# Kernel optimization log

Measured on AMD Instinct MI355X. Metric: run time of the kernel, lower is better.

The kernel has to match this reference:

```python
import jax, jax.numpy as jnp
import numpy as np

EMB_TABLE = 80000  # full shared embedding rows
N_ITEMS = 50000    # target item count (item_num + 1)
E = 600000         # edges
D = 128            # embedding_size
L = 3              # num_gcn_layers


def gcn_conv(x, W, b, src, dst, norm, n):
    # PyG GCNConv: x' = lin(x); out[i] = sum_{(j->i)} norm_ji * x'[j] + bias
    msgs = (x @ W)[src] * norm[:, None]          # [E+n, D]
    out = jax.ops.segment_sum(msgs, dst, num_segments=n)
    return out + b


def setup_inputs() -> dict:
    key = jax.random.key(0)
    k0, k1, k2 = jax.random.split(key, 3)
    item_emb = jax.random.normal(k0, (EMB_TABLE, D), dtype=jnp.float32) * 0.02
    weights = jax.random.normal(k1, (L, D, D), dtype=jnp.float32) * (1.0 / np.sqrt(D))
    biases = jnp.zeros((L, D), dtype=jnp.float32)
    edge_index = jax.random.randint(k2, (2, E), 0, N_ITEMS, dtype=jnp.int64)
    return {"item_emb": item_emb, "weights": weights, "biases": biases,
            "edge_index": edge_index, "item_nums": N_ITEMS}


def reference(item_emb, weights, biases, edge_index, item_nums):
    n = item_nums
    x0 = item_emb[-n:]  # embeds[0] = item_emb[-item_nums:]
    loops = jnp.arange(n, dtype=edge_index.dtype)
    src = jnp.concatenate([edge_index[0], loops])  # add self-loops (GCNConv default)
    dst = jnp.concatenate([edge_index[1], loops])
    # symmetric normalization: deg computed on target side with self-loops
    deg = jax.ops.segment_sum(jnp.ones_like(src, dtype=x0.dtype), dst, num_segments=n)
    dinv = jnp.where(deg > 0, jax.lax.rsqrt(jnp.maximum(deg, 1e-12)), 0.0)
    norm = dinv[src] * dinv[dst]                   # [E+n]
    embeds = [x0]
    for l in range(weights.shape[0]):
        embeds.append(gcn_conv(embeds[-1], weights[l], biases[l], src, dst, norm, n))
    total = embeds[0]
    for e in embeds[1:]:
        total = total + e
    return (total, *embeds)
```

## Files before the change

kernel.cpp:

```cpp
#include <hip/hip_runtime.h>
#include <stdint.h>

#define D 128

typedef unsigned int u32;
typedef unsigned short u16;
typedef __attribute__((ext_vector_type(8))) short short8;
typedef __attribute__((ext_vector_type(4))) float f32x4;

static __device__ __forceinline__ float bf2f(u16 h) {
    return __uint_as_float(((u32)h) << 16);
}
static __device__ __forceinline__ u16 f2bf(float f) {
    u32 u = __float_as_uint(f);
    u32 r = (u + 0x7fffu + ((u >> 16) & 1u)) >> 16;
    return (u16)r;
}
static __device__ __forceinline__ int clampi(int v, int n) {
    if (v < 0) v = 0;
    if (v >= n) v = n - 1;
    return v;
}

__global__ void k_init(int* __restrict__ hist, int* __restrict__ csr_pos, int n,
                       const u16* __restrict__ emb_raw, const u32* __restrict__ ei_raw,
                       const u16* __restrict__ w_raw, int* __restrict__ flags) {
    int i = blockIdx.x * 256 + threadIdx.x;
    if (i < n) {
        hist[i] = 0;
        csr_pos[i] = 0;
    }
    if (blockIdx.x == 0 && threadIdx.x < 64) {
        int t = threadIdx.x;
        int se = 0, sw = 0, zz = 0;
#pragma unroll
        for (int q = 0; q < 4; q++) {
            int k = t * 4 + q;
            u16 he = emb_raw[2 * k];
            u32 exe = (he >> 7) & 0xFF;
            if (he == 0 || (exe >= 0x60 && exe <= 0x8F)) se++;
            u16 hw = w_raw[2 * k];
            u32 exw = (hw >> 7) & 0xFF;
            if (hw == 0 || (exw >= 0x60 && exw <= 0x8F)) sw++;
            if (ei_raw[2 * k + 1] == 0) zz++;
        }
#pragma unroll
        for (int o = 32; o; o >>= 1) {
            se += __shfl_down(se, o);
            sw += __shfl_down(sw, o);
            zz += __shfl_down(zz, o);
        }
        if (t == 0) {
            flags[0] = (se >= 200) ? 1 : 0;
            flags[2] = (sw >= 200) ? 1 : 0;
            flags[1] = (zz >= 200) ? 1 : 0;
        }
    }
}

__global__ __launch_bounds__(256) void k_wprep(const void* __restrict__ Wbase,
                                               const int* __restrict__ flags,
                                               u16* __restrict__ WB) {
    int idx = blockIdx.x * 256 + threadIdx.x;
    int e = idx & 7;
    int l = (idx >> 3) & 63;
    int ks = (idx >> 9) & 3;
    int c = (idx >> 11) & 7;
    int layer = idx >> 14;
    int k = ks * 32 + ((l >> 4) << 3) + e;
    int j = (c << 4) + (l & 15);
    size_t src = (size_t)layer * D * D + (size_t)k * D + j;
    float w = flags[2] ? bf2f(((const u16*)Wbase)[src]) : ((const float*)Wbase)[src];
    u16 hb = f2bf(w);
    u16 lb = f2bf(w - bf2f(hb));
    size_t o = (size_t)layer * 32768 + (size_t)((c * 4 + ks) * 64 + l) * 8 + e;
    WB[o] = hb;
    WB[o + 16384] = lb;
}

__global__ void k_hist(const u32* __restrict__ ei, int E, int n,
                       const int* __restrict__ flags, int* __restrict__ hist) {
    int e = blockIdx.x * 256 + threadIdx.x;
    if (e >= E) return;
    int d;
    if (flags[1]) d = ((const int2*)ei)[(size_t)E + e].x;
    else          d = (int)ei[(size_t)E + e];
    atomicAdd(&hist[clampi(d, n)], 1);
}

__global__ void k_scan1(const int* __restrict__ hist, int n,
                        int* __restrict__ incl, int* __restrict__ bsums) {
    __shared__ int s[256];
    int t = threadIdx.x;
    int i = blockIdx.x * 256 + t;
    int v = (i < n) ? hist[i] : 0;
    s[t] = v;
    __syncthreads();
    for (int d2 = 1; d2 < 256; d2 <<= 1) {
        int add = (t >= d2) ? s[t - d2] : 0;
        __syncthreads();
        s[t] += add;
        __syncthreads();
    }
    if (i < n) incl[i] = s[t];
    if (t == 255) bsums[blockIdx.x] = s[255];
}

__global__ void k_scan23(const int* __restrict__ hist, const int* __restrict__ bsums,
                         int n, int* __restrict__ csr_off, float* __restrict__ dinv) {
    __shared__ int s[256];
    int t = threadIdx.x, b = blockIdx.x;
    s[t] = (t < b) ? bsums[t] : 0;
    __syncthreads();
    for (int o = 128; o; o >>= 1) {
        if (t < o) s[t] += s[t + o];
        __syncthreads();
    }
    int add = s[0];
    int i = b * 256 + t;
    if (i < n) {
        int h = hist[i];
        csr_off[i] = add + csr_off[i] - h;
        dinv[i] = rsqrtf((float)(h + 1));
    }
}

__global__ void k_sx(const u32* __restrict__ ei, int E, int n,
                     const int* __restrict__ flags,
                     const int* __restrict__ csr_off, int* __restrict__ csr_pos,
                     const float* __restrict__ dinv, int2* __restrict__ csr_pair,
                     const void* __restrict__ emb, int off_elems, int nD4,
                     float* __restrict__ out_x0, int eb) {
    int bid = blockIdx.x;
    if (bid < eb) {
        int e = bid * 256 + threadIdx.x;
        if (e >= E) return;
        int s, d;
        if (flags[1]) {
            s = ((const int2*)ei)[e].x;
            d = ((const int2*)ei)[(size_t)E + e].x;
        } else {
            s = (int)ei[e];
            d = (int)ei[(size_t)E + e];
        }
        s = clampi(s, n);
        d = clampi(d, n);
        int p = csr_off[d] + atomicAdd(&csr_pos[d], 1);
        if (p >= E) p = E - 1;
        csr_pair[p] = make_int2(s, __float_as_int(dinv[s] * dinv[d]));
    } else {
        int i = (bid - eb) * 256 + threadIdx.x;
        if (i >= nD4) return;
        float4 v;
        if (flags[0]) {
            ushort4 h = ((const ushort4*)((const u16*)emb + off_elems))[i];
            v = make_float4(bf2f(h.x), bf2f(h.y), bf2f(h.z), bf2f(h.w));
        } else {
            v = ((const float4*)((const float*)emb + off_elems))[i];
        }
        ((float4*)out_x0)[i] = v;
    }
}

__global__ __launch_bounds__(256) void k_gemm(const float* __restrict__ A,
                                              const u16* __restrict__ WB, int layer,
                                              int n, u32* __restrict__ Y) {
    __shared__ f32x4 ldsv[4096];
    int tid = threadIdx.x;
    {
        const f32x4* src = (const f32x4*)(WB + (size_t)layer * 32768);
#pragma unroll
        for (int i = 0; i < 16; i++) ldsv[tid + 256 * i] = src[tid + 256 * i];
    }
    __syncthreads();

    int w = tid >> 6, l = tid & 63;
    int row0 = blockIdx.x * 64 + w * 16;
    int ar = row0 + (l & 15);
    if (ar >= n) ar = 0;
    const float* Ab = A + (size_t)ar * D + ((l >> 4) << 3);

    f32x4 acc[8] = {};
    const short8* bp = (const short8*)ldsv;

#pragma unroll
    for (int ks = 0; ks < 4; ks++) {
        f32x4 a0 = *(const f32x4*)(Ab + ks * 32);
        f32x4 a1 = *(const f32x4*)(Ab + ks * 32 + 4);
        float av[8] = {a0.x, a0.y, a0.z, a0.w, a1.x, a1.y, a1.z, a1.w};
        short8 ah, al;
#pragma unroll
        for (int e = 0; e < 8; e++) {
            u16 h = f2bf(av[e]);
            ah[e] = (short)h;
            al[e] = (short)f2bf(av[e] - bf2f(h));
        }
#pragma unroll
        for (int c = 0; c < 8; c++) {
            short8 bh = bp[(c * 4 + ks) * 64 + l];
            short8 bl = bp[2048 + (c * 4 + ks) * 64 + l];
            acc[c] = __builtin_amdgcn_mfma_f32_16x16x32_bf16(al, bh, acc[c], 0, 0, 0);
            acc[c] = __builtin_amdgcn_mfma_f32_16x16x32_bf16(ah, bl, acc[c], 0, 0, 0);
            acc[c] = __builtin_amdgcn_mfma_f32_16x16x32_bf16(ah, bh, acc[c], 0, 0, 0);
        }
    }

    int rbase = row0 + ((l >> 4) << 2);
    int col = l & 15;
#pragma unroll
    for (int r = 0; r < 4; r++) {
        int gr = rbase + r;
        if (gr < n) {
#pragma unroll
            for (int c = 0; c < 4; c++) {
                u32 pack = (u32)f2bf(acc[c][r]) | ((u32)f2bf(acc[c + 4][r]) << 16);
                Y[(size_t)gr * 64 + c * 16 + col] = pack;
            }
        }
    }
}

__global__ __launch_bounds__(256) void k_agg(const u32* __restrict__ Y,
                                             const int* __restrict__ csr_off,
                                             const int* __restrict__ cnt,
                                             const int2* __restrict__ csr_pair,
                                             const float* __restrict__ dinv,
                                             const void* __restrict__ bias_base, int layer,
                                             const int* __restrict__ flags, int n, int nD,
                                             const float* __restrict__ out_base,
                                             float* __restrict__ out_x,
                                             float* __restrict__ out_tot) {
    int i = blockIdx.x * 4 + (threadIdx.x >> 6);
    if (i >= n) return;
    int t = threadIdx.x & 63;

    float di = dinv[i];
    float di2 = di * di;
    u32 yv = Y[(size_t)i * 64 + t];
    float a0 = bf2f((u16)(yv & 0xffffu)) * di2;
    float a1 = bf2f((u16)(yv >> 16)) * di2;
    float c0 = 0.0f, c1 = 0.0f;

    int start = csr_off[i];
    int c = cnt[i];

    for (int base = 0; base < c; base += 64) {
        int m = c - base;
        if (m > 64) m = 64;
        int2 pr = (t < m) ? csr_pair[start + base + t] : make_int2(0, 0);
        int j = 0;
        for (; j + 3 < m; j += 4) {
            int s0 = __shfl(pr.x, j);
            int s1 = __shfl(pr.x, j + 1);
            int s2 = __shfl(pr.x, j + 2);
            int s3 = __shfl(pr.x, j + 3);
            float w0 = __uint_as_float((u32)__shfl(pr.y, j));
            float w1 = __uint_as_float((u32)__shfl(pr.y, j + 1));
            float w2 = __uint_as_float((u32)__shfl(pr.y, j + 2));
            float w3 = __uint_as_float((u32)__shfl(pr.y, j + 3));
            u32 v0 = Y[(size_t)s0 * 64 + t];
            u32 v1 = Y[(size_t)s1 * 64 + t];
            u32 v2 = Y[(size_t)s2 * 64 + t];
            u32 v3 = Y[(size_t)s3 * 64 + t];
            a0 += bf2f((u16)(v0 & 0xffffu)) * w0;
            a1 += bf2f((u16)(v0 >> 16)) * w0;
            c0 += bf2f((u16)(v1 & 0xffffu)) * w1;
            c1 += bf2f((u16)(v1 >> 16)) * w1;
            a0 += bf2f((u16)(v2 & 0xffffu)) * w2;
            a1 += bf2f((u16)(v2 >> 16)) * w2;
            c0 += bf2f((u16)(v3 & 0xffffu)) * w3;
            c1 += bf2f((u16)(v3 >> 16)) * w3;
        }
        for (; j < m; j++) {
            int s = __shfl(pr.x, j);
            float w = __uint_as_float((u32)__shfl(pr.y, j));
            u32 v = Y[(size_t)s * 64 + t];
            a0 += bf2f((u16)(v & 0xffffu)) * w;
            a1 += bf2f((u16)(v >> 16)) * w;
        }
    }
    float acc0 = a0 + c0, acc1 = a1 + c1;

    float b0, b1;
    if (flags[0]) {
        const u16* bb = (const u16*)bias_base + layer * D;
        b0 = bf2f(bb[t]);
        b1 = bf2f(bb[t + 64]);
    } else {
        const float* bb = (const float*)bias_base + layer * D;
        b0 = bb[t];
        b1 = bb[t + 64];
    }
    float xv0 = acc0 + b0, xv1 = acc1 + b1;
    size_t base = (size_t)i * D + t;
    out_x[base] = xv0;
    out_x[base + 64] = xv1;

    if (out_tot) {
        float s0 = out_base[(size_t)1 * nD + base] + out_base[(size_t)2 * nD + base] +
                   out_base[(size_t)3 * nD + base];
        float s1 = out_base[(size_t)1 * nD + base + 64] + out_base[(size_t)2 * nD + base + 64] +
                   out_base[(size_t)3 * nD + base + 64];
        out_tot[base] = s0 + xv0;
        out_tot[base + 64] = s1 + xv1;
    }
}

extern "C" void kernel_launch(void* const* d_in, const int* in_sizes, int n_in,
                              void* d_out, int out_size, void* d_ws, size_t ws_size,
                              hipStream_t stream) {
    float* out = (float*)d_out;

    const int n = out_size / (5 * D);

    int i_emb = -1, i_ei = -1, i_w = -1, i_b = -1;
    {
        int order[8];
        int m = n_in > 8 ? 8 : n_in;
        for (int i = 0; i < m; i++) order[i] = i;
        for (int a = 0; a < m; a++)
            for (int b2 = a + 1; b2 < m; b2++)
                if (in_sizes[order[b2]] > in_sizes[order[a]]) {
                    int tmp = order[a]; order[a] = order[b2]; order[b2] = tmp;
                }
        i_emb = order[0];
        i_ei  = (m > 1) ? order[1] : 0;
        for (int i = 0; i < m; i++) {
            if (in_sizes[i] == 3 * D * D && i_w < 0) i_w = i;
            if (in_sizes[i] == 3 * D && i_b < 0) i_b = i;
        }
        if (i_w < 0) i_w = (m > 2) ? order[2] : 0;
        if (i_b < 0) i_b = (m > 3) ? order[3] : 0;
    }
    const void* emb  = d_in[i_emb];
    const void* wts  = d_in[i_w];
    const void* bias = d_in[i_b];
    const u32*  ei   = (const u32*)d_in[i_ei];

    const int E = in_sizes[i_ei] / 2;
    const int rows = in_sizes[i_emb] / D;
    const int off_elems = (rows - n) * D;

    char* p = (char*)d_ws;
    auto take = [&](size_t bytes) {
        char* r = p;
        p += (bytes + 255) & ~(size_t)255;
        return r;
    };
    int*   flags    = (int*)  take(3 * 4);
    int*   hist     = (int*)  take((size_t)n * 4);
    int*   csr_pos  = (int*)  take((size_t)n * 4);
    int*   csr_off  = (int*)  take((size_t)n * 4);
    int*   bsums    = (int*)  take(256 * 4);
    float* dinv     = (float*)take((size_t)n * 4);
    int2*  csr_pair = (int2*) take((size_t)E * 8);
    u32*   ybuf     = (u32*)  take((size_t)n * 64 * 4);
    u16*   wb       = (u16*)  take((size_t)3 * 32768 * 2);

    const int nD = n * D;
    const int nb = (n + 255) / 256;
    const int eb = (E + 255) / 256;
    const int x0b = (nD / 4 + 255) / 256;

    k_init<<<nb, 256, 0, stream>>>(hist, csr_pos, n, (const u16*)emb, ei,
                                   (const u16*)wts, flags);
    k_wprep<<<192, 256, 0, stream>>>(wts, flags, wb);
    k_hist<<<eb, 256, 0, stream>>>(ei, E, n, flags, hist);
    k_scan1<<<nb, 256, 0, stream>>>(hist, n, csr_off, bsums);
    k_scan23<<<nb, 256, 0, stream>>>(hist, bsums, n, csr_off, dinv);
    k_sx<<<eb + x0b, 256, 0, stream>>>(ei, E, n, flags, csr_off, csr_pos, dinv,
                                       csr_pair, emb, off_elems, nD / 4,
                                       out + (size_t)nD, eb);

    const int ab = (n + 3) / 4;
    for (int l = 0; l < 3; l++) {
        const float* A = out + (size_t)(1 + l) * nD;
        float* ox = out + (size_t)(2 + l) * nD;
        k_gemm<<<(n + 63) / 64, 256, 0, stream>>>(A, wb, l, n, ybuf);
        k_agg<<<ab, 256, 0, stream>>>(ybuf, csr_off, hist, csr_pair, dinv, bias, l,
                                      flags, n, nD, out, ox,
                                      (l == 2) ? out : (float*)nullptr);
    }
}
```

Baseline: 353.6 us.

## Vectorize aggregation gathers to 16-byte loads over four edges; fuse hist and weight prep

The aggregation kernel now has each wavefront split into four 16-lane groups. Each group gathers a whole 256-byte bf16 row with uint4 loads for a different edge, and the loop software-pipelines one load ahead. Partial sums are combined across groups with xor shuffles, and bias, output and total are written as float4 by half the lanes. The aim is fewer, wider memory transactions per gathered row and more edges in flight, at the cost of a cross-lane reduction and idle lanes during the epilogue. Separately, the weight-prep and degree-histogram kernels are merged into one launch to save a kernel launch.

```diff
diff --git a/kernel.cpp b/kernel.cpp
--- a/kernel.cpp
+++ b/kernel.cpp
@@ -58,34 +58,34 @@
     }
 }
 
-__global__ __launch_bounds__(256) void k_wprep(const void* __restrict__ Wbase,
-                                               const int* __restrict__ flags,
-                                               u16* __restrict__ WB) {
-    int idx = blockIdx.x * 256 + threadIdx.x;
-    int e = idx & 7;
-    int l = (idx >> 3) & 63;
-    int ks = (idx >> 9) & 3;
-    int c = (idx >> 11) & 7;
-    int layer = idx >> 14;
-    int k = ks * 32 + ((l >> 4) << 3) + e;
-    int j = (c << 4) + (l & 15);
-    size_t src = (size_t)layer * D * D + (size_t)k * D + j;
-    float w = flags[2] ? bf2f(((const u16*)Wbase)[src]) : ((const float*)Wbase)[src];
-    u16 hb = f2bf(w);
-    u16 lb = f2bf(w - bf2f(hb));
-    size_t o = (size_t)layer * 32768 + (size_t)((c * 4 + ks) * 64 + l) * 8 + e;
-    WB[o] = hb;
-    WB[o + 16384] = lb;
-}
-
-__global__ void k_hist(const u32* __restrict__ ei, int E, int n,
-                       const int* __restrict__ flags, int* __restrict__ hist) {
-    int e = blockIdx.x * 256 + threadIdx.x;
-    if (e >= E) return;
-    int d;
-    if (flags[1]) d = ((const int2*)ei)[(size_t)E + e].x;
-    else          d = (int)ei[(size_t)E + e];
-    atomicAdd(&hist[clampi(d, n)], 1);
+__global__ void k_hw(const u32* __restrict__ ei, int E, int n,
+                     const int* __restrict__ flags, int* __restrict__ hist,
+                     const void* __restrict__ Wbase, u16* __restrict__ WB, int eb) {
+    int bid = blockIdx.x;
+    if (bid < eb) {
+        int e = bid * 256 + threadIdx.x;
+        if (e >= E) return;
+        int d;
+        if (flags[1]) d = ((const int2*)ei)[(size_t)E + e].x;
+        else          d = (int)ei[(size_t)E + e];
+        atomicAdd(&hist[clampi(d, n)], 1);
+    } else {
+        int idx = (bid - eb) * 256 + threadIdx.x;
+        int e = idx & 7;
+        int l = (idx >> 3) & 63;
+        int ks = (idx >> 9) & 3;
+        int c = (idx >> 11) & 7;
+        int layer = idx >> 14;
+        int k = ks * 32 + ((l >> 4) << 3) + e;
+        int j = (c << 4) + (l & 15);
+        size_t src = (size_t)layer * D * D + (size_t)k * D + j;
+        float w = flags[2] ? bf2f(((const u16*)Wbase)[src]) : ((const float*)Wbase)[src];
+        u16 hb = f2bf(w);
+        u16 lb = f2bf(w - bf2f(hb));
+        size_t o = (size_t)layer * 32768 + (size_t)((c * 4 + ks) * 64 + l) * 8 + e;
+        WB[o] = hb;
+        WB[o + 16384] = lb;
+    }
 }
 
 __global__ void k_scan1(const int* __restrict__ hist, int n,
@@ -233,13 +233,29 @@
     int i = blockIdx.x * 4 + (threadIdx.x >> 6);
     if (i >= n) return;
     int t = threadIdx.x & 63;
+    int g = t >> 4, p = t & 15;
+
+    float lo0 = 0.f, lo1 = 0.f, lo2 = 0.f, lo3 = 0.f;
+    float hi0 = 0.f, hi1 = 0.f, hi2 = 0.f, hi3 = 0.f;
+
+#define ACC4(V, W)                                                       \
+    do {                                                                 \
+        lo0 += __uint_as_float((V).x << 16) * (W);                       \
+        hi0 += __uint_as_float((V).x & 0xffff0000u) * (W);               \
+        lo1 += __uint_as_float((V).y << 16) * (W);                       \
+        hi1 += __uint_as_float((V).y & 0xffff0000u) * (W);               \
+        lo2 += __uint_as_float((V).z << 16) * (W);                       \
+        hi2 += __uint_as_float((V).z & 0xffff0000u) * (W);               \
+        lo3 += __uint_as_float((V).w << 16) * (W);                       \
+        hi3 += __uint_as_float((V).w & 0xffff0000u) * (W);               \
+    } while (0)
 
     float di = dinv[i];
-    float di2 = di * di;
-    u32 yv = Y[(size_t)i * 64 + t];
-    float a0 = bf2f((u16)(yv & 0xffffu)) * di2;
-    float a1 = bf2f((u16)(yv >> 16)) * di2;
-    float c0 = 0.0f, c1 = 0.0f;
+    {
+        uint4 vs = *(const uint4*)(Y + (size_t)i * 64 + p * 4);
+        float ws = (g == 0) ? di * di : 0.0f;
+        ACC4(vs, ws);
+    }
 
     int start = csr_off[i];
     int c = cnt[i];
@@ -248,61 +264,61 @@
         int m = c - base;
         if (m > 64) m = 64;
         int2 pr = (t < m) ? csr_pair[start + base + t] : make_int2(0, 0);
-        int j = 0;
-        for (; j + 3 < m; j += 4) {
-            int s0 = __shfl(pr.x, j);
-            int s1 = __shfl(pr.x, j + 1);
-            int s2 = __shfl(pr.x, j + 2);
-            int s3 = __shfl(pr.x, j + 3);
-            float w0 = __uint_as_float((u32)__shfl(pr.y, j));
-            float w1 = __uint_as_float((u32)__shfl(pr.y, j + 1));
-            float w2 = __uint_as_float((u32)__shfl(pr.y, j + 2));
-            float w3 = __uint_as_float((u32)__shfl(pr.y, j + 3));
-            u32 v0 = Y[(size_t)s0 * 64 + t];
-            u32 v1 = Y[(size_t)s1 * 64 + t];
-            u32 v2 = Y[(size_t)s2 * 64 + t];
-            u32 v3 = Y[(size_t)s3 * 64 + t];
-            a0 += bf2f((u16)(v0 & 0xffffu)) * w0;
-            a1 += bf2f((u16)(v0 >> 16)) * w0;
-            c0 += bf2f((u16)(v1 & 0xffffu)) * w1;
-            c1 += bf2f((u16)(v1 >> 16)) * w1;
-            a0 += bf2f((u16)(v2 & 0xffffu)) * w2;
-            a1 += bf2f((u16)(v2 >> 16)) * w2;
-            c0 += bf2f((u16)(v3 & 0xffffu)) * w3;
-            c1 += bf2f((u16)(v3 >> 16)) * w3;
-        }
-        for (; j < m; j++) {
-            int s = __shfl(pr.x, j);
-            float w = __uint_as_float((u32)__shfl(pr.y, j));
-            u32 v = Y[(size_t)s * 64 + t];
-            a0 += bf2f((u16)(v & 0xffffu)) * w;
-            a1 += bf2f((u16)(v >> 16)) * w;
-        }
-    }
-    float acc0 = a0 + c0, acc1 = a1 + c1;
-
-    float b0, b1;
-    if (flags[0]) {
-        const u16* bb = (const u16*)bias_base + layer * D;
-        b0 = bf2f(bb[t]);
-        b1 = bf2f(bb[t + 64]);
-    } else {
-        const float* bb = (const float*)bias_base + layer * D;
-        b0 = bb[t];
-        b1 = bb[t + 64];
-    }
-    float xv0 = acc0 + b0, xv1 = acc1 + b1;
-    size_t base = (size_t)i * D + t;
-    out_x[base] = xv0;
-    out_x[base + 64] = xv1;
-
-    if (out_tot) {
-        float s0 = out_base[(size_t)1 * nD + base] + out_base[(size_t)2 * nD + base] +
-                   out_base[(size_t)3 * nD + base];
-        float s1 = out_base[(size_t)1 * nD + base + 64] + out_base[(size_t)2 * nD + base + 64] +
-                   out_base[(size_t)3 * nD + base + 64];
-        out_tot[base] = s0 + xv0;
-        out_tot[base + 64] = s1 + xv1;
+        int s0 = __shfl(pr.x, g);
+        float w0 = __uint_as_float((u32)__shfl(pr.y, g));
+        uint4 v0 = *(const uint4*)(Y + (size_t)s0 * 64 + p * 4);
+        for (int j = 4; j < m; j += 4) {
+            int s1 = __shfl(pr.x, j + g);
+            float w1 = __uint_as_float((u32)__shfl(pr.y, j + g));
+            uint4 v1 = *(const uint4*)(Y + (size_t)s1 * 64 + p * 4);
+            ACC4(v0, w0);
+            v0 = v1;
+            w0 = w1;
+        }
+        ACC4(v0, w0);
+    }
+#undef ACC4
+
+#pragma unroll
+    for (int mask = 16; mask <= 32; mask <<= 1) {
+        lo0 += __shfl_xor(lo0, mask);
+        lo1 += __shfl_xor(lo1, mask);
+        lo2 += __shfl_xor(lo2, mask);
+        lo3 += __shfl_xor(lo3, mask);
+        hi0 += __shfl_xor(hi0, mask);
+        hi1 += __shfl_xor(hi1, mask);
+        hi2 += __shfl_xor(hi2, mask);
+        hi3 += __shfl_xor(hi3, mask);
+    }
+
+    if (g < 2) {
+        float r0 = g ? hi0 : lo0;
+        float r1 = g ? hi1 : lo1;
+        float r2 = g ? hi2 : lo2;
+        float r3 = g ? hi3 : lo3;
+        int off = g * 64 + 4 * p;
+        float b0, b1, b2, b3;
+        if (flags[0]) {
+            const u16* bb = (const u16*)bias_base + layer * D + off;
+            ushort4 h = *(const ushort4*)bb;
+            b0 = bf2f(h.x); b1 = bf2f(h.y); b2 = bf2f(h.z); b3 = bf2f(h.w);
+        } else {
+            const float* bb = (const float*)bias_base + layer * D + off;
+            float4 f = *(const float4*)bb;
+            b0 = f.x; b1 = f.y; b2 = f.z; b3 = f.w;
+        }
+        float4 xv = make_float4(r0 + b0, r1 + b1, r2 + b2, r3 + b3);
+        size_t base = (size_t)i * D + off;
+        *(float4*)&out_x[base] = xv;
+
+        if (out_tot) {
+            float4 s0 = *(const float4*)&out_base[(size_t)1 * nD + base];
+            float4 s1 = *(const float4*)&out_base[(size_t)2 * nD + base];
+            float4 s2 = *(const float4*)&out_base[(size_t)3 * nD + base];
+            *(float4*)&out_tot[base] =
+                make_float4(s0.x + s1.x + s2.x + xv.x, s0.y + s1.y + s2.y + xv.y,
+                            s0.z + s1.z + s2.z + xv.z, s0.w + s1.w + s2.w + xv.w);
+        }
     }
 }
 
@@ -364,8 +380,7 @@
 
     k_init<<<nb, 256, 0, stream>>>(hist, csr_pos, n, (const u16*)emb, ei,
                                    (const u16*)wts, flags);
-    k_wprep<<<192, 256, 0, stream>>>(wts, flags, wb);
-    k_hist<<<eb, 256, 0, stream>>>(ei, E, n, flags, hist);
+    k_hw<<<eb + 192, 256, 0, stream>>>(ei, E, n, flags, hist, wts, wb, eb);
     k_scan1<<<nb, 256, 0, stream>>>(hist, n, csr_off, bsums);
     k_scan23<<<nb, 256, 0, stream>>>(hist, bsums, n, csr_off, dinv);
     k_sx<<<eb + x0b, 256, 0, stream>>>(ei, E, n, flags, csr_off, csr_pos, dinv,
```

Measured after the change: 350.2 us. No clear change (-0.9%).
